# Kernel optimization log

Hardware: AMD Instinct MI355X
Metric: run time of the kernel (lower is better)

## Reference

```python
import jax, jax.numpy as jnp
import numpy as np

T, N, F = 8, 384, 32
N_TYPE, MAX_NODE, IN_DIM, HID = 3, 130, 256, 64  # IN_DIM = T*F
C = IN_DIM // 2  # graph channels = conv channels = 128 = MAX_NODE - 2


def setup_inputs():
    key = jax.random.key(0)
    ks = jax.random.split(key, 10)
    V = jax.random.normal(ks[0], (1, T, N, F + 1), dtype=jnp.float32)
    types = (jnp.arange(N) % N_TYPE + 1).astype(jnp.float32)  # exactly 128 nodes per type
    V = V.at[..., -1].set(types)
    graph = jax.random.normal(ks[1], (C, N, N), dtype=jnp.float32)
    u = lambda k, s: jax.random.uniform(k, s, jnp.float32, -0.1, 0.1)
    return dict(
        V=V,
        graph=graph,
        node_type=(jnp.arange(N) % N_TYPE + 1).astype(jnp.int32),
        ex=1,
        lin0_w=u(ks[2], (MAX_NODE // 2, MAX_NODE)),
        lin0_b=u(ks[3], (MAX_NODE // 2,)),
        att_lin_w=u(ks[4], (N_TYPE, HID, IN_DIM)),
        att_lin_b=u(ks[5], (N_TYPE, HID)),
        agg=jax.random.uniform(ks[6], (N_TYPE, 2 * HID, 1), jnp.float32, -1.0, 1.0),
        pl=u(ks[7], (1,)),
        conv2_w=u(ks[8], (C, C, 2, 2)),
        conv2_b=u(ks[9], (C,)),
    )


def _forward(V, graph, lin0_w, lin0_b, att_lin_w, att_lin_b, agg, pl, conv2_w, conv2_b):
    Vs = V[0]                                   # [T, N, F+1]
    t_vec = Vs[0, :, -1].astype(jnp.int32)      # [N], node types in 1..n_type
    feats = jnp.transpose(Vs[:, :, :-1], (1, 0, 2)).reshape(N, T * F)  # [N, T*F]

    # per-type stable gather + zero-pad to MAX_NODE, then node-dim Linear(max_node -> max_node//2)
    def per_type(k):
        mask = t_vec == (k + 1)
        idx = jnp.argsort(jnp.logical_not(mask), stable=True)[:MAX_NODE]
        vk = feats[idx] * mask[idx][:, None].astype(feats.dtype)   # [MAX_NODE, D]
        vk = (vk.T @ lin0_w.T + lin0_b).T                          # [MAX_NODE//2, D]
        return vk

    v = jax.vmap(per_type)(jnp.arange(N_TYPE))  # [n_type, M2, D]

    # TypeAttentionLayer per type idx: linear -> concat with row idx -> agg matmul -> lrelu -> max over nodes -> softmax over types
    def att_layer(Wk, bk, aggk, k):
        x = jnp.einsum('tnd,hd->tnh', v, Wk) + bk               # [n_type, M2, H]
        xi = jnp.take(x, k, axis=0)                             # [M2, H]
        x2 = jnp.concatenate([x, jnp.broadcast_to(xi, x.shape)], axis=-1)  # [n_type, M2, 2H]
        s = jax.nn.leaky_relu(jnp.einsum('tnh,h->tn', x2, aggk[:, 0]))     # slope 0.01, as torch
        return jax.nn.softmax(jnp.max(s, axis=1), axis=0)       # [n_type]

    A = jax.vmap(att_layer)(att_lin_w, att_lin_b, agg, jnp.arange(N_TYPE))  # [n_type, n_type]

    # scatter per-type-pair scores into adjacency: att_mx[i,j] = A[t_i-1, t_j-1]
    att_mx = A[t_vec[:, None] - 1, t_vec[None, :] - 1]          # [N, N]
    wei = graph * att_mx                                        # ablation == 0

    # nb_cnn: zero-pad bottom/right by MAX_NODE - len(graph) = MAX_NODE - C, then valid 2x2 convs back to NxN
    pad = MAX_NODE - C
    wg = jnp.pad(wei, ((0, 0), (0, pad), (0, pad)))
    for _ in range(pad):
        wg = jax.lax.conv_general_dilated(
            wg[None], conv2_w, (1, 1), 'VALID',
            dimension_numbers=('NCHW', 'OIHW', 'NCHW'))[0] + conv2_b[:, None, None]

    out = pl * wg + graph                                       # univ == 2
    return jax.nn.relu(out)                                     # sparse


def reference(V, graph, node_type, ex, lin0_w, lin0_b, att_lin_w, att_lin_b, agg, pl, conv2_w, conv2_b):
    if not ex:
        return None
    return _forward(V, graph, lin0_w, lin0_b, att_lin_w, att_lin_b, agg, pl, conv2_w, conv2_b)
```

## Files before the change

kernel.cpp:

```cpp
#include <hip/hip_runtime.h>

typedef __attribute__((ext_vector_type(8))) short bf16x8;
typedef __attribute__((ext_vector_type(4))) float f32x4;
typedef unsigned int u32;
typedef unsigned short u16;
typedef unsigned long long u64;

#define S0 384
#define PLANE0 (384 * 384)
#define XR 386
#define XROWB ((size_t)XR * 256)

__device__ __forceinline__ u16 bfr(float f) {
    u32 b = __float_as_uint(f);
    b += 0x7fff + ((b >> 16) & 1);
    return (u16)(b >> 16);
}

__global__ __launch_bounds__(256) void k_prep_v(
        const float* __restrict__ cw, const float* __restrict__ cb,
        u16* __restrict__ Ebf2, float* __restrict__ beff,
        const float* __restrict__ V,
        const float* __restrict__ lin0_w, const float* __restrict__ lin0_b,
        float* __restrict__ v_out) {
    const int tid = threadIdx.x;
    if (blockIdx.x < 128) {
        int o = blockIdx.x, i = tid & 127;
        __shared__ float4 Wo[128];
        __shared__ float red[128];
        Wo[i] = *(const float4*)(cw + (size_t)(o * 128 + i) * 4);
        __syncthreads();
        float a9[9];
#pragma unroll
        for (int q = 0; q < 9; ++q) a9[q] = 0.f;
        for (int m = 0; m < 128; ++m) {
            float4 w1 = *(const float4*)(cw + (size_t)(m * 128 + i) * 4);
            float4 w2 = Wo[m];
            a9[0] += w2.x * w1.x;
            a9[1] += w2.x * w1.y + w2.y * w1.x;
            a9[2] += w2.y * w1.y;
            a9[3] += w2.x * w1.z + w2.z * w1.x;
            a9[4] += w2.x * w1.w + w2.y * w1.z + w2.z * w1.y + w2.w * w1.x;
            a9[5] += w2.y * w1.w + w2.w * w1.y;
            a9[6] += w2.z * w1.z;
            a9[7] += w2.z * w1.w + w2.w * w1.z;
            a9[8] += w2.w * w1.w;
        }
        int icg = i >> 5, el = i & 31;
#pragma unroll
        for (int q = 0; q < 9; ++q)
            Ebf2[(size_t)((q * 4 + icg) * 128 + o) * 32 + el] = bfr(a9[q]);
        float4 wo = Wo[i];
        red[i] = cb[i] * (wo.x + wo.y + wo.z + wo.w);
        __syncthreads();
        for (int s = 64; s > 0; s >>= 1) {
            if (tid < 128 && i < s) red[i] += red[i + s];
            __syncthreads();
        }
        if (tid == 0) beff[o] = cb[o] + red[0];
    } else {
        int blk = blockIdx.x - 128;
        int k = blk / 65, m = blk % 65;
        int d = tid;
        int t = d >> 5, f = d & 31;
        const float* vbase = V + (size_t)t * 384 * 33 + f;
        float acc = lin0_b[m];
        for (int r = 0; r < 128; ++r) {
            float w = lin0_w[m * 130 + r];
            acc += w * vbase[(3 * r + k) * 33];
        }
        v_out[(size_t)blk * 256 + d] = acc;
    }
}

__global__ void k_att(const float* __restrict__ v,
                      const float* __restrict__ att_w,
                      const float* __restrict__ att_b,
                      const float* __restrict__ agg,
                      float* __restrict__ A_out) {
    int k = blockIdx.x;
    int tid = threadIdx.x;
    __shared__ float wv1[256], wv2[256];
    __shared__ float sbuf[3][65];
    __shared__ float Ck_s;
    __shared__ float sm[3];
    {
        int d = tid;
        float a1 = 0.f, a2 = 0.f;
        for (int h = 0; h < 64; ++h) {
            float w = att_w[((size_t)(k * 64 + h)) * 256 + d];
            a1 += agg[k * 128 + h] * w;
            a2 += agg[k * 128 + 64 + h] * w;
        }
        wv1[d] = a1;
        wv2[d] = a2;
    }
    if (tid == 0) {
        float c = 0.f;
        for (int h = 0; h < 64; ++h)
            c += (agg[k * 128 + h] + agg[k * 128 + 64 + h]) * att_b[k * 64 + h];
        Ck_s = c;
    }
    __syncthreads();
    if (tid < 195) {
        int t = tid / 65, m = tid % 65;
        const float* vt = v + ((size_t)(t * 65 + m)) * 256;
        const float* vk = v + ((size_t)(k * 65 + m)) * 256;
        float s = Ck_s;
        for (int d = 0; d < 256; ++d)
            s += vt[d] * wv1[d] + vk[d] * wv2[d];
        s = s > 0.f ? s : 0.01f * s;
        sbuf[t][m] = s;
    }
    __syncthreads();
    if (tid < 3) {
        float mx = sbuf[tid][0];
        for (int m = 1; m < 65; ++m) mx = fmaxf(mx, sbuf[tid][m]);
        sm[tid] = mx;
    }
    __syncthreads();
    if (tid == 0) {
        float mx = fmaxf(sm[0], fmaxf(sm[1], sm[2]));
        float e0 = __expf(sm[0] - mx), e1 = __expf(sm[1] - mx), e2 = __expf(sm[2] - mx);
        float inv = 1.f / (e0 + e1 + e2);
        A_out[k * 3 + 0] = e0 * inv;
        A_out[k * 3 + 1] = e1 * inv;
        A_out[k * 3 + 2] = e2 * inv;
    }
}

__global__ __launch_bounds__(256) void k_pack(
        const float* __restrict__ graph,
        const float* __restrict__ A9g,
        u16* __restrict__ X) {
    __shared__ u16 T[128 * 136];
    const int tid = threadIdx.x;
    const int xt = blockIdx.x, y = blockIdx.y;
    const int x0p = xt * 128;
    const uint4 z = {0u, 0u, 0u, 0u};

    if (y >= 384) {
        int nunits = (xt == 2) ? 130 * 16 : 128 * 16;
        for (int u = tid; u < nunits; u += 256) {
            int x = x0p + (u >> 4), j = u & 15;
            *(uint4*)((char*)X + ((size_t)y * XR + x) * 256 + j * 16) = z;
        }
        return;
    }

    const int ic0 = (tid & 31) * 4;
    const int xc = tid >> 5;
    float ar[3];
    ar[0] = A9g[(y % 3) * 3 + 0];
    ar[1] = A9g[(y % 3) * 3 + 1];
    ar[2] = A9g[(y % 3) * 3 + 2];
    const int m0 = (x0p + xc * 16) % 3;
    float facs[3];
    facs[0] = ar[m0];
    facs[1] = ar[m0 + 1 == 3 ? 0 : m0 + 1];
    facs[2] = ar[m0 + 2 >= 3 ? m0 - 1 : m0 + 2];

    float vals[4][16];
#pragma unroll
    for (int ici = 0; ici < 4; ++ici) {
        const float* g = graph + (size_t)(ic0 + ici) * PLANE0 + (size_t)y * S0 + x0p + xc * 16;
#pragma unroll
        for (int q = 0; q < 4; ++q) {
            float4 f = *(const float4*)(g + q * 4);
            vals[ici][q * 4 + 0] = f.x;
            vals[ici][q * 4 + 1] = f.y;
            vals[ici][q * 4 + 2] = f.z;
            vals[ici][q * 4 + 3] = f.w;
        }
    }
#pragma unroll
    for (int e = 0; e < 16; ++e) {
        float f = facs[e % 3];
        int x = xc * 16 + e;
        u16 q0 = bfr(vals[0][e] * f);
        u16 q1 = bfr(vals[1][e] * f);
        u16 q2 = bfr(vals[2][e] * f);
        u16 q3 = bfr(vals[3][e] * f);
        u64 w = (u64)q0 | ((u64)q1 << 16) | ((u64)q2 << 32) | ((u64)q3 << 48);
        *(u64*)(T + x * 136 + ic0) = w;
    }
    __syncthreads();

#pragma unroll
    for (int i = 0; i < 8; ++i) {
        int u = tid + 256 * i;
        int x = u >> 4, j = u & 15;
        int oct = j ^ (x & 15);
        uint4 w = *(const uint4*)(T + x * 136 + oct * 8);
        *(uint4*)((char*)X + ((size_t)y * XR + x0p + x) * 256 + j * 16) = w;
    }
    if (xt == 2 && tid < 32) {
        int x = 384 + (tid >> 4), j = tid & 15;
        *(uint4*)((char*)X + ((size_t)y * XR + x) * 256 + j * 16) = z;
    }
}

__global__ __launch_bounds__(256, 3) void k_conv9(
        const u16* __restrict__ X,
        const short* __restrict__ Ebf2,
        const float* __restrict__ beff,
        const float* __restrict__ pl,
        const float* __restrict__ graph,
        float* __restrict__ out) {
    const int tid = threadIdx.x;
    const int lane = tid & 63, wave = tid >> 6;
    const int l15 = lane & 15, l16 = lane >> 4;

    const int phys = blockIdx.x;
    const int logical = (phys & 7) * 144 + (phys >> 3);
    const int bx = logical % 6, by = logical / 6;
    const int x0 = bx * 64, y0 = by * 2;
    const int mh = wave & 1, rh = wave >> 1;
    const int ocbase = mh * 64;

    const char* Xbase = (const char*)X + ((size_t)(y0 + rh) * XR + x0) * 256;

#define ALOAD(dst, s) {                                                        \
        const short* Ap = Ebf2 + ((size_t)((s) * 128 + ocbase + l15) << 5)     \
                          + l16 * 8;                                           \
        dst[0] = *(const bf16x8*)(Ap);                                         \
        dst[1] = *(const bf16x8*)(Ap + 512);                                   \
        dst[2] = *(const bf16x8*)(Ap + 1024);                                  \
        dst[3] = *(const bf16x8*)(Ap + 1536); }

#define BOFF(s, n) ((size_t)(((s) >> 2) / 3) * XROWB                           \
        + ((l15 + (n) * 16 + ((s) >> 2) % 3) << 8)                             \
        + (((((s) & 3) * 4 + l16) ^ ((l15 + (n) * 16 + ((s) >> 2) % 3) & 15)) << 4))

#define BLOAD(dst, s) {                                                        \
        dst[0] = *(const bf16x8*)(Xbase + BOFF(s, 0));                         \
        dst[1] = *(const bf16x8*)(Xbase + BOFF(s, 1));                         \
        dst[2] = *(const bf16x8*)(Xbase + BOFF(s, 2));                         \
        dst[3] = *(const bf16x8*)(Xbase + BOFF(s, 3)); }

    bf16x8 ap[2][4], bp[2][4];
    ALOAD(ap[0], 0); BLOAD(bp[0], 0);
    ALOAD(ap[1], 1); BLOAD(bp[1], 1);

    f32x4 acc[4][4];
#pragma unroll
    for (int a = 0; a < 4; ++a)
#pragma unroll
        for (int b = 0; b < 4; ++b)
            acc[a][b] = (f32x4){0.f, 0.f, 0.f, 0.f};

#pragma unroll
    for (int s = 0; s < 36; ++s) {
        const int cur = s & 1;
        __builtin_amdgcn_s_setprio(1);
#pragma unroll
        for (int n = 0; n < 4; ++n) {
            acc[0][n] = __builtin_amdgcn_mfma_f32_16x16x32_bf16(ap[cur][0], bp[cur][n], acc[0][n], 0, 0, 0);
            acc[1][n] = __builtin_amdgcn_mfma_f32_16x16x32_bf16(ap[cur][1], bp[cur][n], acc[1][n], 0, 0, 0);
            acc[2][n] = __builtin_amdgcn_mfma_f32_16x16x32_bf16(ap[cur][2], bp[cur][n], acc[2][n], 0, 0, 0);
            acc[3][n] = __builtin_amdgcn_mfma_f32_16x16x32_bf16(ap[cur][3], bp[cur][n], acc[3][n], 0, 0, 0);
        }
        __builtin_amdgcn_s_setprio(0);
        if (s + 2 < 36) { ALOAD(ap[cur], s + 2); BLOAD(bp[cur], s + 2); }
    }
#undef ALOAD
#undef BLOAD
#undef BOFF

    const float plv = pl[0];
    const int yy = y0 + rh;
#pragma unroll
    for (int m = 0; m < 4; ++m) {
#pragma unroll
        for (int r4 = 0; r4 < 4; ++r4) {
            const int oc = ocbase + m * 16 + l16 * 4 + r4;
            const float bias = beff[oc];
            const float* grow = graph + (size_t)oc * PLANE0 + (size_t)yy * S0 + x0;
            float* orow = out + (size_t)oc * PLANE0 + (size_t)yy * S0 + x0;
#pragma unroll
            for (int n = 0; n < 4; ++n) {
                const int xx = n * 16 + l15;
                float v = plv * (acc[m][n][r4] + bias) + grow[xx];
                orow[xx] = v > 0.f ? v : 0.f;
            }
        }
    }
}

extern "C" void kernel_launch(void* const* d_in, const int* in_sizes, int n_in,
                              void* d_out, int out_size, void* d_ws, size_t ws_size,
                              hipStream_t stream) {
    (void)in_sizes; (void)n_in; (void)out_size; (void)ws_size;
    const float* V      = (const float*)d_in[0];
    const float* graph  = (const float*)d_in[1];
    const float* lin0_w = (const float*)d_in[4];
    const float* lin0_b = (const float*)d_in[5];
    const float* att_w  = (const float*)d_in[6];
    const float* att_b  = (const float*)d_in[7];
    const float* agg    = (const float*)d_in[8];
    const float* pl     = (const float*)d_in[9];
    const float* cw     = (const float*)d_in[10];
    const float* cb     = (const float*)d_in[11];
    float* out = (float*)d_out;

    char* ws = (char*)d_ws;
    float* v_ws  = (float*)ws;
    float* A_ws  = (float*)(ws + 200704);
    u16*   Ebf2  = (u16*)(ws + 200768);
    float* beff  = (float*)(ws + 495680);
    u16*   X     = (u16*)(ws + 496192);

    k_prep_v<<<323, 256, 0, stream>>>(cw, cb, Ebf2, beff, V, lin0_w, lin0_b, v_ws);
    k_att<<<3, 256, 0, stream>>>(v_ws, att_w, att_b, agg, A_ws);
    k_pack<<<dim3(3, 386), 256, 0, stream>>>(graph, A_ws, X);
    k_conv9<<<1152, 256, 0, stream>>>(
        X, (const short*)Ebf2, beff, pl, graph, out);
}
```

Before: 175.5 us.

## Stage conv input tile in LDS via global_load_lds and retile conv to 48-wide

The main conv kernel now copies its whole input patch (4 rows x 52 columns) into shared memory with asynchronous global-to-LDS loads, then reads B fragments from LDS instead of global memory. The tile width drops from 64 to 48 columns, giving 1536 blocks. The weight (A) prefetch depth goes up to four stages, and the pack kernel's swizzle is changed to an 8-way XOR that matches the new LDS read pattern. The attention kernel also gets float4-vectorised dot products and unrolling. This trades repeated global/L2 reads of overlapping rows for about 52KB of LDS per block, which may limit occupancy.

```diff
diff --git a/kernel.cpp b/kernel.cpp
--- a/kernel.cpp
+++ b/kernel.cpp
@@ -10,6 +10,10 @@
 #define PLANE0 (384 * 384)
 #define XR 386
 #define XROWB ((size_t)XR * 256)
+
+#define GLOAD_LDS(g, l) __builtin_amdgcn_global_load_lds( \
+    (const __attribute__((address_space(1))) void*)(g),   \
+    (__attribute__((address_space(3))) void*)(l), 16, 0, 0)
 
 __device__ __forceinline__ u16 bfr(float f) {
     u32 b = __float_as_uint(f);
@@ -80,13 +84,14 @@
                       float* __restrict__ A_out) {
     int k = blockIdx.x;
     int tid = threadIdx.x;
-    __shared__ float wv1[256], wv2[256];
+    __shared__ __align__(16) float wv1[256], wv2[256];
     __shared__ float sbuf[3][65];
     __shared__ float Ck_s;
     __shared__ float sm[3];
     {
         int d = tid;
         float a1 = 0.f, a2 = 0.f;
+#pragma unroll 8
         for (int h = 0; h < 64; ++h) {
             float w = att_w[((size_t)(k * 64 + h)) * 256 + d];
             a1 += agg[k * 128 + h] * w;
@@ -104,11 +109,17 @@
     __syncthreads();
     if (tid < 195) {
         int t = tid / 65, m = tid % 65;
-        const float* vt = v + ((size_t)(t * 65 + m)) * 256;
-        const float* vk = v + ((size_t)(k * 65 + m)) * 256;
+        const float4* vt = (const float4*)(v + ((size_t)(t * 65 + m)) * 256);
+        const float4* vk = (const float4*)(v + ((size_t)(k * 65 + m)) * 256);
+        const float4* w1 = (const float4*)wv1;
+        const float4* w2 = (const float4*)wv2;
         float s = Ck_s;
-        for (int d = 0; d < 256; ++d)
-            s += vt[d] * wv1[d] + vk[d] * wv2[d];
+#pragma unroll 8
+        for (int d = 0; d < 64; ++d) {
+            float4 a = vt[d], b = w1[d], c = vk[d], e = w2[d];
+            s += a.x * b.x + a.y * b.y + a.z * b.z + a.w * b.w;
+            s += c.x * e.x + c.y * e.y + c.z * e.z + c.w * e.w;
+        }
         s = s > 0.f ? s : 0.01f * s;
         sbuf[t][m] = s;
     }
@@ -190,7 +201,7 @@
     for (int i = 0; i < 8; ++i) {
         int u = tid + 256 * i;
         int x = u >> 4, j = u & 15;
-        int oct = j ^ (x & 15);
+        int oct = (j & 8) | ((j & 7) ^ (x & 7));
         uint4 w = *(const uint4*)(T + x * 136 + oct * 8);
         *(uint4*)((char*)X + ((size_t)y * XR + x0p + x) * 256 + j * 16) = w;
     }
@@ -207,18 +218,28 @@
         const float* __restrict__ pl,
         const float* __restrict__ graph,
         float* __restrict__ out) {
+    __shared__ __align__(16) char Bt[53248];
     const int tid = threadIdx.x;
     const int lane = tid & 63, wave = tid >> 6;
     const int l15 = lane & 15, l16 = lane >> 4;
 
     const int phys = blockIdx.x;
-    const int logical = (phys & 7) * 144 + (phys >> 3);
-    const int bx = logical % 6, by = logical / 6;
-    const int x0 = bx * 64, y0 = by * 2;
+    const int logical = (phys & 7) * 192 + (phys >> 3);
+    const int bx = logical & 7, by = logical >> 3;
+    const int x0 = bx * 48, y0 = by * 2;
     const int mh = wave & 1, rh = wave >> 1;
     const int ocbase = mh * 64;
 
-    const char* Xbase = (const char*)X + ((size_t)(y0 + rh) * XR + x0) * 256;
+    {
+        const char* gsrc = (const char*)X + ((size_t)y0 * XR + x0) * 256;
+#pragma unroll
+        for (int i = 0; i < 13; ++i) {
+            int u = tid + i * 256;
+            int r = u / 832;
+            int off = (u - r * 832) * 16;
+            GLOAD_LDS(gsrc + (size_t)r * XROWB + off, Bt + u * 16);
+        }
+    }
 
 #define ALOAD(dst, s) {                                                        \
         const short* Ap = Ebf2 + ((size_t)((s) * 128 + ocbase + l15) << 5)     \
@@ -228,44 +249,48 @@
         dst[2] = *(const bf16x8*)(Ap + 1024);                                  \
         dst[3] = *(const bf16x8*)(Ap + 1536); }
 
-#define BOFF(s, n) ((size_t)(((s) >> 2) / 3) * XROWB                           \
+    bf16x8 ap[4][4];
+    ALOAD(ap[0], 0); ALOAD(ap[1], 1); ALOAD(ap[2], 2); ALOAD(ap[3], 3);
+
+    __syncthreads();
+
+    f32x4 acc[4][3];
+#pragma unroll
+    for (int a = 0; a < 4; ++a)
+#pragma unroll
+        for (int b = 0; b < 3; ++b)
+            acc[a][b] = (f32x4){0.f, 0.f, 0.f, 0.f};
+
+#define BADDR(s, n) (Bt + (rh + ((s) >> 2) / 3) * 13312                        \
         + ((l15 + (n) * 16 + ((s) >> 2) % 3) << 8)                             \
-        + (((((s) & 3) * 4 + l16) ^ ((l15 + (n) * 16 + ((s) >> 2) % 3) & 15)) << 4))
-
-#define BLOAD(dst, s) {                                                        \
-        dst[0] = *(const bf16x8*)(Xbase + BOFF(s, 0));                         \
-        dst[1] = *(const bf16x8*)(Xbase + BOFF(s, 1));                         \
-        dst[2] = *(const bf16x8*)(Xbase + BOFF(s, 2));                         \
-        dst[3] = *(const bf16x8*)(Xbase + BOFF(s, 3)); }
-
-    bf16x8 ap[2][4], bp[2][4];
-    ALOAD(ap[0], 0); BLOAD(bp[0], 0);
-    ALOAD(ap[1], 1); BLOAD(bp[1], 1);
-
-    f32x4 acc[4][4];
-#pragma unroll
-    for (int a = 0; a < 4; ++a)
-#pragma unroll
-        for (int b = 0; b < 4; ++b)
-            acc[a][b] = (f32x4){0.f, 0.f, 0.f, 0.f};
+        + (((((s) & 3) * 4 + l16) >> 3) << 7)                                  \
+        + ((((((s) & 3) * 4 + l16) & 7) ^ ((l15 + (n) * 16 + ((s) >> 2) % 3) & 7)) << 4))
+
+    bf16x8 bp[2][3];
+#pragma unroll
+    for (int n = 0; n < 3; ++n) bp[0][n] = *(const bf16x8*)BADDR(0, n);
 
 #pragma unroll
     for (int s = 0; s < 36; ++s) {
         const int cur = s & 1;
+        if (s < 35) {
+#pragma unroll
+            for (int n = 0; n < 3; ++n)
+                bp[cur ^ 1][n] = *(const bf16x8*)BADDR(s + 1, n);
+        }
         __builtin_amdgcn_s_setprio(1);
 #pragma unroll
-        for (int n = 0; n < 4; ++n) {
-            acc[0][n] = __builtin_amdgcn_mfma_f32_16x16x32_bf16(ap[cur][0], bp[cur][n], acc[0][n], 0, 0, 0);
-            acc[1][n] = __builtin_amdgcn_mfma_f32_16x16x32_bf16(ap[cur][1], bp[cur][n], acc[1][n], 0, 0, 0);
-            acc[2][n] = __builtin_amdgcn_mfma_f32_16x16x32_bf16(ap[cur][2], bp[cur][n], acc[2][n], 0, 0, 0);
-            acc[3][n] = __builtin_amdgcn_mfma_f32_16x16x32_bf16(ap[cur][3], bp[cur][n], acc[3][n], 0, 0, 0);
+        for (int n = 0; n < 3; ++n) {
+            acc[0][n] = __builtin_amdgcn_mfma_f32_16x16x32_bf16(ap[s & 3][0], bp[cur][n], acc[0][n], 0, 0, 0);
+            acc[1][n] = __builtin_amdgcn_mfma_f32_16x16x32_bf16(ap[s & 3][1], bp[cur][n], acc[1][n], 0, 0, 0);
+            acc[2][n] = __builtin_amdgcn_mfma_f32_16x16x32_bf16(ap[s & 3][2], bp[cur][n], acc[2][n], 0, 0, 0);
+            acc[3][n] = __builtin_amdgcn_mfma_f32_16x16x32_bf16(ap[s & 3][3], bp[cur][n], acc[3][n], 0, 0, 0);
         }
         __builtin_amdgcn_s_setprio(0);
-        if (s + 2 < 36) { ALOAD(ap[cur], s + 2); BLOAD(bp[cur], s + 2); }
+        if (s + 4 < 36) ALOAD(ap[s & 3], s + 4);
     }
 #undef ALOAD
-#undef BLOAD
-#undef BOFF
+#undef BADDR
 
     const float plv = pl[0];
     const int yy = y0 + rh;
@@ -278,7 +303,7 @@
             const float* grow = graph + (size_t)oc * PLANE0 + (size_t)yy * S0 + x0;
             float* orow = out + (size_t)oc * PLANE0 + (size_t)yy * S0 + x0;
 #pragma unroll
-            for (int n = 0; n < 4; ++n) {
+            for (int n = 0; n < 3; ++n) {
                 const int xx = n * 16 + l15;
                 float v = plv * (acc[m][n][r4] + bias) + grow[xx];
                 orow[xx] = v > 0.f ? v : 0.f;
@@ -313,6 +338,6 @@
     k_prep_v<<<323, 256, 0, stream>>>(cw, cb, Ebf2, beff, V, lin0_w, lin0_b, v_ws);
     k_att<<<3, 256, 0, stream>>>(v_ws, att_w, att_b, agg, A_ws);
     k_pack<<<dim3(3, 386), 256, 0, stream>>>(graph, A_ws, X);
-    k_conv9<<<1152, 256, 0, stream>>>(
+    k_conv9<<<1536, 256, 0, stream>>>(
         X, (const short*)Ebf2, beff, pl, graph, out);
 }
```

Result: faster. 141.6 us (-19.3%).
